# Kernel tuning notes

Measured on AMD Instinct MI355X. Metric: run time of the kernel, lower is better.

Reference implementation:

```python
import jax, jax.numpy as jnp
import numpy as np

B, S, H, NH = 2, 2048, 1024, 16
HD = H // NH  # head_dim = 64


def setup_inputs() -> dict:
    key = jax.random.key(0)
    k1, k2, k3, k4, k5 = jax.random.split(key, 5)
    hidden_states = jax.random.normal(k1, (B, S, H), dtype=jnp.float32)
    # additive causal mask: 0 on/below diagonal, -1e9 above
    causal = jnp.tril(jnp.ones((S, S), dtype=jnp.bool_))
    attention_mask = jnp.where(causal, 0.0, -1e9).astype(jnp.float32)[None, None, :, :]
    scale = 0.02
    Wq = jax.random.normal(k2, (H, H), dtype=jnp.float32) * scale
    Wk = jax.random.normal(k3, (H, H), dtype=jnp.float32) * scale
    Wv = jax.random.normal(k4, (H, H), dtype=jnp.float32) * scale
    Wo = jax.random.normal(k5, (H, H), dtype=jnp.float32) * scale
    return {"hidden_states": hidden_states, "attention_mask": attention_mask,
            "Wq": Wq, "Wk": Wk, "Wv": Wv, "Wo": Wo}


def reference(hidden_states, attention_mask, Wq, Wk, Wv, Wo):
    b, s, _ = hidden_states.shape
    # nn.Linear: y = x @ W.T
    q = (hidden_states @ Wq.T).reshape(b, s, NH, HD).transpose(0, 2, 1, 3)  # [B,NH,S,HD]
    k = (hidden_states @ Wk.T).reshape(b, s, NH, HD).transpose(0, 2, 1, 3)
    v = (hidden_states @ Wv.T).reshape(b, s, NH, HD).transpose(0, 2, 1, 3)
    scores = jnp.einsum('bhqd,bhkd->bhqk', q, k) / jnp.sqrt(jnp.float32(HD))
    scores = scores + attention_mask
    attn = jax.nn.softmax(scores, axis=-1)
    out = jnp.einsum('bhqk,bhkd->bhqd', attn, v)  # [B,NH,S,HD]
    out = out.transpose(0, 2, 1, 3).reshape(b, s, H)
    return out @ Wo.T
```

## Files before the change

kernel.cpp:

```cpp
#include <hip/hip_runtime.h>
#include <hip/hip_bf16.h>

#define B_   2
#define S_   2048
#define H_   1024
#define NH_  16
#define HD_  64
#define MTOT 4096
#define KD   1024

typedef __attribute__((ext_vector_type(4)))  float    f32x4;
typedef __attribute__((ext_vector_type(16))) float    f32x16;
typedef __attribute__((ext_vector_type(8)))  short    bf16x8;
typedef __attribute__((ext_vector_type(2)))  unsigned u32x2;
typedef __attribute__((ext_vector_type(4)))  unsigned u32x4;

__device__ inline short f2bf(float x) {
    union { float f; unsigned u; } v; v.f = x;
    unsigned r = v.u + 0x7fffu + ((v.u >> 16) & 1u);
    return (short)(r >> 16);
}
__device__ inline unsigned pk2(float lo, float hi) {
    return (unsigned)(unsigned short)f2bf(lo) | ((unsigned)(unsigned short)f2bf(hi) << 16);
}
__device__ inline unsigned cvtpk(float lo, float hi) {
    unsigned r;
    asm("v_cvt_pk_bf16_f32 %0, %1, %2" : "=v"(r) : "v"(lo), "v"(hi));
    return r;
}
__device__ inline float max3f(float a, float b, float c) {
    float r;
    asm("v_max3_f32 %0, %1, %2, %3" : "=v"(r) : "v"(a), "v"(b), "v"(c));
    return r;
}
__device__ inline void gload16(const void* g, void* l) {
    __builtin_amdgcn_global_load_lds(
        (const __attribute__((address_space(1))) unsigned*)g,
        (__attribute__((address_space(3))) unsigned*)l, 16, 0, 0);
}

__global__ __launch_bounds__(256) void cvt_x(const float* __restrict__ x,
                                             unsigned* __restrict__ xb) {
    const size_t i = ((size_t)blockIdx.x * 256 + threadIdx.x) * 8;
    const f32x4 a = *(const f32x4*)(x + i);
    const f32x4 b = *(const f32x4*)(x + i + 4);
    u32x4 p;
    p[0] = pk2(a[0], a[1]); p[1] = pk2(a[2], a[3]);
    p[2] = pk2(b[0], b[1]); p[3] = pk2(b[2], b[3]);
    *(u32x4*)(xb + i / 2) = p;
}

__global__ __launch_bounds__(256) void wcvt(const float* __restrict__ W0,
                                            const float* __restrict__ W1,
                                            const float* __restrict__ W2,
                                            const float* __restrict__ W3,
                                            unsigned* __restrict__ wb) {
    const float* W = (blockIdx.y == 0) ? W0 : (blockIdx.y == 1) ? W1
                   : (blockIdx.y == 2) ? W2 : W3;
    const size_t i = ((size_t)blockIdx.x * 256 + threadIdx.x) * 8;
    const f32x4 a = *(const f32x4*)(W + i);
    const f32x4 b = *(const f32x4*)(W + i + 4);
    u32x4 p;
    p[0] = pk2(a[0], a[1]); p[1] = pk2(a[2], a[3]);
    p[2] = pk2(b[0], b[1]); p[3] = pk2(b[2], b[3]);
    *(u32x4*)(wb + (size_t)blockIdx.y * (H_ * KD / 2) + i / 2) = p;
}

template <int MODE>
__global__ __launch_bounds__(256) void gemm_m97(const short* __restrict__ A,
                                                const short* __restrict__ Wb,
                                                short* __restrict__ outb,
                                                float* __restrict__ outf) {
    __shared__ short Sm[128 * 128];
    short* As = Sm;
    short* Bs = Sm + 8192;

    const int tid = threadIdx.x, wave = tid >> 6, lane = tid & 63;
    const int wm = (wave >> 1) * 64, wn = (wave & 1) * 64;
    const int m0 = blockIdx.x * 128;

    int n0, widx;
    if constexpr (MODE == 0) {
        widx = blockIdx.y >> 3;
        n0 = (blockIdx.y & 7) * 128;
    } else {
        widx = 0;
        n0 = blockIdx.y * 128;
    }
    const short* W = Wb + (size_t)widx * H_ * KD;

    f32x4 acc[4][4] = {};

    for (int k0 = 0; k0 < KD; k0 += 64) {
#pragma unroll
        for (int c = 0; c < 4; ++c) {
            const int lin = wave * 4096 + c * 1024 + lane * 16;
            const int row = lin >> 7;
            const int col = (lin & 127) ^ ((row & 7) << 4);
            gload16(A + (size_t)(m0 + row) * KD + k0 + (col >> 1),
                    (char*)As + wave * 4096 + c * 1024);
            gload16(W + (size_t)(n0 + row) * KD + k0 + (col >> 1),
                    (char*)Bs + wave * 4096 + c * 1024);
        }
        __syncthreads();

#pragma unroll
        for (int ks = 0; ks < 2; ++ks) {
            bf16x8 af[4], bf[4];
#pragma unroll
            for (int i = 0; i < 4; ++i) {
                const int row = wm + i * 16 + (lane & 15);
                af[i] = *(const bf16x8*)((char*)As + row * 128 +
                        ((ks * 64 + (lane >> 4) * 16) ^ ((row & 7) << 4)));
            }
#pragma unroll
            for (int j = 0; j < 4; ++j) {
                const int row = wn + j * 16 + (lane & 15);
                bf[j] = *(const bf16x8*)((char*)Bs + row * 128 +
                        ((ks * 64 + (lane >> 4) * 16) ^ ((row & 7) << 4)));
            }
#pragma unroll
            for (int i = 0; i < 4; ++i)
#pragma unroll
                for (int j = 0; j < 4; ++j)
                    acc[i][j] = __builtin_amdgcn_mfma_f32_16x16x32_bf16(af[i], bf[j], acc[i][j], 0, 0, 0);
        }
        __syncthreads();
    }

    if constexpr (MODE == 0) {
#pragma unroll
        for (int i = 0; i < 4; ++i)
#pragma unroll
            for (int j = 0; j < 4; ++j)
#pragma unroll
                for (int r = 0; r < 4; ++r) {
                    const int mi = wm + i * 16 + (lane >> 4) * 4 + r;
                    const int ni = wn + j * 16 + (lane & 15);
                    const int byt = (mi * 256 + ni * 2) ^ ((mi & 7) << 4);
                    *(short*)((char*)Sm + byt) = f2bf(acc[i][j][r]);
                }
        __syncthreads();
        const int row = tid >> 1, half = tid & 1;
        const int m = m0 + row, bb = m >> 11, s = m & 2047;
        const int hh = (n0 >> 6) + half;
        short* dst = outb + (size_t)widx * MTOT * H_ +
                     (((size_t)(bb * NH_ + hh)) * S_ + s) * HD_;
#pragma unroll
        for (int k = 0; k < 8; ++k) {
            const int byt = (row * 256 + half * 128 + k * 16) ^ ((row & 7) << 4);
            *(bf16x8*)(dst + k * 8) = *(const bf16x8*)((char*)Sm + byt);
        }
    } else {
#pragma unroll
        for (int i = 0; i < 4; ++i)
#pragma unroll
            for (int j = 0; j < 4; ++j)
#pragma unroll
                for (int r = 0; r < 4; ++r) {
                    const int m = m0 + wm + i * 16 + (lane >> 4) * 4 + r;
                    const int n = n0 + wn + j * 16 + (lane & 15);
                    outf[(size_t)m * H_ + n] = acc[i][j][r];
                }
    }
}

__global__ __launch_bounds__(512, 4) void flash3(const short* __restrict__ Qb,
                                                 const short* __restrict__ Kb,
                                                 const short* __restrict__ Vb,
                                                 short* __restrict__ Ob) {
    const int bx = blockIdx.x;
    const int hi = bx >> 8, u = bx & 255;
    const int h = u >> 4, tq = u & 15;
    const int qt = hi ? (15 - tq) : tq;
    const int b  = hi;

    const int tid = threadIdx.x, wave = tid >> 6, lane = tid & 63;
    const int qg = wave & 3, half = wave >> 2;
    const int th = tid & 255;
    const int q0 = qt * 128;
    const int qw0 = q0 + qg * 32;
    const size_t hoff = ((size_t)(b * NH_ + h)) * S_ * HD_;
    const short* Q = Qb + hoff;
    const short* K = Kb + hoff;
    const short* V = Vb + hoff;

    __shared__ short Ks[2][2][4096];
    __shared__ short Vt[2][2][4096];

    const int ql = lane & 31;
    const int hh = lane >> 5;

    bf16x8 qf[4];
#pragma unroll
    for (int ds = 0; ds < 4; ++ds)
        qf[ds] = *(const bf16x8*)(Q + (size_t)(qw0 + ql) * HD_ + ds * 16 + hh * 8);

    f32x16 ot[2] = {};
    float mrun = -1e30f, lrun = 0.f;
    const float c2 = 0.18033688011112042f;

    const int kk = (th & 31) * 2, d0v = (th >> 5) * 8;
    bf16x8 vr0, vr1;
    auto stageK = [&](int kt, int buf) {
#pragma unroll
        for (int c = 0; c < 2; ++c) {
            const int lin = qg * 2048 + c * 1024 + lane * 16;
            const int row = lin >> 7;
            const int col = (lin & 127) ^ ((row & 7) << 4);
            gload16(K + (size_t)(kt * 64 + row) * HD_ + (col >> 1),
                    (char*)Ks[half][buf] + qg * 2048 + c * 1024);
        }
    };
    auto loadV = [&](int kt) {
        vr0 = *(const bf16x8*)(V + (size_t)(kt * 64 + kk) * HD_ + d0v);
        vr1 = *(const bf16x8*)(V + (size_t)(kt * 64 + kk + 1) * HD_ + d0v);
    };
    auto writeV = [&](int buf) {
#pragma unroll
        for (int i = 0; i < 8; ++i) {
            const int d = d0v + i;
            const int byt = d * 128 + kk * 2;
            *(unsigned*)((char*)Vt[half][buf] + (byt ^ ((d & 7) << 4))) =
                (unsigned)(unsigned short)vr0[i] | ((unsigned)(unsigned short)vr1[i] << 16);
        }
    };

    const int niter = qt + 1;
    const int ktbase = half ? (qt + 1) : 0;

    stageK(ktbase, 0);
    loadV(ktbase);
    writeV(0);
    __syncthreads();

    int cur = 0;
    for (int it = 0; it < niter; ++it) {
        const int kt = ktbase + it;
        const bool pre = (it + 1 < niter);
        if (pre) { stageK(kt + 1, cur ^ 1); loadV(kt + 1); }

        if (kt * 64 <= qw0 + 31) {
            const bool need_mask = (kt * 64 + 63) > qw0;

            f32x16 st[2] = {};
            __builtin_amdgcn_s_setprio(1);
#pragma unroll
            for (int t = 0; t < 2; ++t)
#pragma unroll
                for (int ds = 0; ds < 4; ++ds) {
                    const int row = t * 32 + ql;
                    const bf16x8 kf = *(const bf16x8*)((char*)Ks[half][cur] + row * 128 +
                            ((ds * 32 + hh * 16) ^ ((row & 7) << 4)));
                    st[t] = __builtin_amdgcn_mfma_f32_32x32x16_bf16(kf, qf[ds], st[t], 0, 0, 0);
                }
            __builtin_amdgcn_s_setprio(0);

            float sraw[32];
#pragma unroll
            for (int t = 0; t < 2; ++t)
#pragma unroll
                for (int r = 0; r < 16; ++r) {
                    float v = st[t][r];
                    if (need_mask) {
                        const int key = kt * 64 + t * 32 + (r & 3) + 8 * (r >> 2) + 4 * hh;
                        if (key > qw0 + ql) v = -1e30f;
                    }
                    sraw[t * 16 + r] = v;
                }

            float ma = fmaxf(sraw[0], sraw[1]);
            float mb = fmaxf(sraw[2], sraw[3]);
#pragma unroll
            for (int i = 4; i < 32; i += 4) {
                ma = max3f(ma, sraw[i],     sraw[i + 1]);
                mb = max3f(mb, sraw[i + 2], sraw[i + 3]);
            }
            const float pmax = fmaxf(fmaxf(ma, mb), __shfl_xor(fmaxf(ma, mb), 32, 64));

            if (!__all((pmax - mrun) <= 44.36f)) {
                const float mnew = fmaxf(mrun, pmax);
                const float corr = exp2f((mrun - mnew) * c2);
                mrun = mnew;
                lrun *= corr;
#pragma unroll
                for (int dt = 0; dt < 2; ++dt)
#pragma unroll
                    for (int r = 0; r < 16; ++r) ot[dt][r] *= corr;
            }
            const float mc = mrun * c2;

            float p[32];
#pragma unroll
            for (int i = 0; i < 32; ++i) p[i] = exp2f(fmaf(sraw[i], c2, -mc));
            float ts[16];
#pragma unroll
            for (int i = 0; i < 16; ++i) ts[i] = p[i] + p[i + 16];
#pragma unroll
            for (int stp = 8; stp >= 1; stp >>= 1)
#pragma unroll
                for (int i = 0; i < 8; ++i)
                    if (i < stp) ts[i] += ts[i + stp];
            lrun += ts[0] + __shfl_xor(ts[0], 32, 64);

#pragma unroll
            for (int ks = 0; ks < 4; ++ks) {
                const int t = ks >> 1, rb = (ks & 1) * 8;
                const unsigned a0 = cvtpk(p[t * 16 + rb + 0], p[t * 16 + rb + 1]);
                const unsigned a1 = cvtpk(p[t * 16 + rb + 2], p[t * 16 + rb + 3]);
                const unsigned a2 = cvtpk(p[t * 16 + rb + 4], p[t * 16 + rb + 5]);
                const unsigned a3 = cvtpk(p[t * 16 + rb + 6], p[t * 16 + rb + 7]);
                const unsigned s0 = __shfl_xor(a0, 32, 64);
                const unsigned s1 = __shfl_xor(a1, 32, 64);
                const unsigned s2 = __shfl_xor(a2, 32, 64);
                const unsigned s3 = __shfl_xor(a3, 32, 64);
                u32x4 pw;
                pw[0] = hh ? s2 : a0;
                pw[1] = hh ? s3 : a1;
                pw[2] = hh ? a2 : s0;
                pw[3] = hh ? a3 : s1;
                const bf16x8 pf = __builtin_bit_cast(bf16x8, pw);
                __builtin_amdgcn_s_setprio(1);
#pragma unroll
                for (int dt = 0; dt < 2; ++dt) {
                    const int row = dt * 32 + ql;
                    const bf16x8 vf = *(const bf16x8*)((char*)Vt[half][cur] + row * 128 +
                            ((ks * 32 + hh * 16) ^ ((row & 7) << 4)));
                    ot[dt] = __builtin_amdgcn_mfma_f32_32x32x16_bf16(vf, pf, ot[dt], 0, 0, 0);
                }
                __builtin_amdgcn_s_setprio(0);
            }
        }

        if (pre) writeV(cur ^ 1);
        __syncthreads();
        cur ^= 1;
    }

    float* Osh = (float*)Ks;
    float* Msh = (float*)Vt;
    const int swz = (lane & 7) << 2;

    if (half == 1) {
        float* dst = Osh + ((size_t)qg * 64 + lane) * 32;
#pragma unroll
        for (int dt = 0; dt < 2; ++dt)
#pragma unroll
            for (int g4 = 0; g4 < 4; ++g4) {
                f32x4 t;
                t[0] = ot[dt][g4 * 4 + 0]; t[1] = ot[dt][g4 * 4 + 1];
                t[2] = ot[dt][g4 * 4 + 2]; t[3] = ot[dt][g4 * 4 + 3];
                *(f32x4*)(dst + ((dt * 16 + g4 * 4) ^ swz)) = t;
            }
        Msh[(qg * 64 + lane) * 2 + 0] = mrun;
        Msh[(qg * 64 + lane) * 2 + 1] = lrun;
    }
    __syncthreads();

    if (half == 0) {
        const float* src = Osh + ((size_t)qg * 64 + lane) * 32;
        const float mB = Msh[(qg * 64 + lane) * 2 + 0];
        const float lB = Msh[(qg * 64 + lane) * 2 + 1];
        const float m  = fmaxf(mrun, mB);
        const float al = exp2f((mrun - m) * c2);
        const float be = exp2f((mB   - m) * c2);
        const float inv = 1.f / (al * lrun + be * lB);
        const float ai = al * inv, bi = be * inv;

        short* orow = Ob + ((size_t)(b * S_) + q0 + qg * 32 + ql) * H_ + h * HD_;
#pragma unroll
        for (int dt = 0; dt < 2; ++dt)
#pragma unroll
            for (int g4 = 0; g4 < 4; ++g4) {
                const f32x4 ob = *(const f32x4*)(src + ((dt * 16 + g4 * 4) ^ swz));
                const int dbase = dt * 32 + 8 * g4 + 4 * hh;
                u32x2 w;
                w[0] = cvtpk(ot[dt][g4 * 4 + 0] * ai + ob[0] * bi,
                             ot[dt][g4 * 4 + 1] * ai + ob[1] * bi);
                w[1] = cvtpk(ot[dt][g4 * 4 + 2] * ai + ob[2] * bi,
                             ot[dt][g4 * 4 + 3] * ai + ob[3] * bi);
                *(u32x2*)(orow + dbase) = w;
            }
    }
}

extern "C" void kernel_launch(void* const* d_in, const int* in_sizes, int n_in,
                              void* d_out, int out_size, void* d_ws, size_t ws_size,
                              hipStream_t stream) {
    const float* x  = (const float*)d_in[0];
    const float* Wq = (const float*)d_in[2];
    const float* Wk = (const float*)d_in[3];
    const float* Wv = (const float*)d_in[4];
    const float* Wo = (const float*)d_in[5];
    float* out = (float*)d_out;

    short* qkv = (short*)d_ws;
    short* xb  = qkv + (size_t)3 * MTOT * H_;
    short* wb  = xb + (size_t)MTOT * H_;

    cvt_x<<<2048, 256, 0, stream>>>(x, (unsigned*)xb);
    wcvt<<<dim3(512, 4), 256, 0, stream>>>(Wq, Wk, Wv, Wo, (unsigned*)wb);

    gemm_m97<0><<<dim3(32, 24), 256, 0, stream>>>(xb, wb, qkv, nullptr);

    flash3<<<dim3(512), 512, 0, stream>>>(
        qkv, qkv + (size_t)MTOT * H_, qkv + (size_t)2 * MTOT * H_, xb);

    gemm_m97<1><<<dim3(32, 8), 256, 0, stream>>>(
        xb, wb + (size_t)3 * H_ * KD, nullptr, out);
}
```

Before: 153.0 us.

## Interleave KV tiles between wave halves instead of contiguous ranges

The two halves of the workgroup previously each walked a contiguous range of KV tiles (first half from 0, second from qt+1). Now each iteration stages a pair of adjacent tiles with all 512 threads cooperating, and the halves take even and odd tiles. The goal is to keep the causal-masked diagonal work balanced between halves and to share the staging load across all waves. It changes which tiles each half covers and how many it visits, so both halves now hit masked and skipped tiles near the diagonal.

```diff
diff --git a/kernel.cpp b/kernel.cpp
--- a/kernel.cpp
+++ b/kernel.cpp
@@ -165,7 +165,7 @@
     }
 }
 
-__global__ __launch_bounds__(512, 4) void flash3(const short* __restrict__ Qb,
+__global__ __launch_bounds__(512, 4) void flash4(const short* __restrict__ Qb,
                                                  const short* __restrict__ Kb,
                                                  const short* __restrict__ Vb,
                                                  short* __restrict__ Ob) {
@@ -176,8 +176,7 @@
     const int b  = hi;
 
     const int tid = threadIdx.x, wave = tid >> 6, lane = tid & 63;
-    const int qg = wave & 3, half = wave >> 2;
-    const int th = tid & 255;
+    const int qg = wave & 3, par = wave >> 2;
     const int q0 = qt * 128;
     const int qw0 = q0 + qg * 32;
     const size_t hoff = ((size_t)(b * NH_ + h)) * S_ * HD_;
@@ -200,46 +199,52 @@
     float mrun = -1e30f, lrun = 0.f;
     const float c2 = 0.18033688011112042f;
 
-    const int kk = (th & 31) * 2, d0v = (th >> 5) * 8;
-    bf16x8 vr0, vr1;
-    auto stageK = [&](int kt, int buf) {
+    auto stagePair = [&](int j) {
+        const int buf = j & 1;
 #pragma unroll
         for (int c = 0; c < 2; ++c) {
-            const int lin = qg * 2048 + c * 1024 + lane * 16;
+            const int chunk = wave * 2 + c;
+            const int pt  = chunk >> 3;
+            const int sub = chunk & 7;
+            const int lin = sub * 1024 + lane * 16;
             const int row = lin >> 7;
             const int col = (lin & 127) ^ ((row & 7) << 4);
-            gload16(K + (size_t)(kt * 64 + row) * HD_ + (col >> 1),
-                    (char*)Ks[half][buf] + qg * 2048 + c * 1024);
+            gload16(K + (size_t)((2 * j + pt) * 64 + row) * HD_ + (col >> 1),
+                    (char*)Ks[pt][buf] + sub * 1024);
         }
     };
-    auto loadV = [&](int kt) {
+    const int vpar = tid >> 8;
+    const int kk = (tid & 31) * 2, d0v = ((tid >> 5) & 7) * 8;
+    bf16x8 vr0, vr1;
+    auto loadV = [&](int j) {
+        const int kt = 2 * j + vpar;
         vr0 = *(const bf16x8*)(V + (size_t)(kt * 64 + kk) * HD_ + d0v);
         vr1 = *(const bf16x8*)(V + (size_t)(kt * 64 + kk + 1) * HD_ + d0v);
     };
-    auto writeV = [&](int buf) {
+    auto writeV = [&](int j) {
+        const int buf = j & 1;
 #pragma unroll
         for (int i = 0; i < 8; ++i) {
             const int d = d0v + i;
             const int byt = d * 128 + kk * 2;
-            *(unsigned*)((char*)Vt[half][buf] + (byt ^ ((d & 7) << 4))) =
+            *(unsigned*)((char*)Vt[vpar][buf] + (byt ^ ((d & 7) << 4))) =
                 (unsigned)(unsigned short)vr0[i] | ((unsigned)(unsigned short)vr1[i] << 16);
         }
     };
 
     const int niter = qt + 1;
-    const int ktbase = half ? (qt + 1) : 0;
-
-    stageK(ktbase, 0);
-    loadV(ktbase);
+
+    stagePair(0);
+    loadV(0);
     writeV(0);
     __syncthreads();
 
-    int cur = 0;
     for (int it = 0; it < niter; ++it) {
-        const int kt = ktbase + it;
         const bool pre = (it + 1 < niter);
-        if (pre) { stageK(kt + 1, cur ^ 1); loadV(kt + 1); }
-
+        if (pre) { stagePair(it + 1); loadV(it + 1); }
+
+        const int kt = 2 * it + par;
+        const int buf = it & 1;
         if (kt * 64 <= qw0 + 31) {
             const bool need_mask = (kt * 64 + 63) > qw0;
 
@@ -250,7 +255,7 @@
 #pragma unroll
                 for (int ds = 0; ds < 4; ++ds) {
                     const int row = t * 32 + ql;
-                    const bf16x8 kf = *(const bf16x8*)((char*)Ks[half][cur] + row * 128 +
+                    const bf16x8 kf = *(const bf16x8*)((char*)Ks[par][buf] + row * 128 +
                             ((ds * 32 + hh * 16) ^ ((row & 7) << 4)));
                     st[t] = __builtin_amdgcn_mfma_f32_32x32x16_bf16(kf, qf[ds], st[t], 0, 0, 0);
                 }
@@ -324,7 +329,7 @@
 #pragma unroll
                 for (int dt = 0; dt < 2; ++dt) {
                     const int row = dt * 32 + ql;
-                    const bf16x8 vf = *(const bf16x8*)((char*)Vt[half][cur] + row * 128 +
+                    const bf16x8 vf = *(const bf16x8*)((char*)Vt[par][buf] + row * 128 +
                             ((ks * 32 + hh * 16) ^ ((row & 7) << 4)));
                     ot[dt] = __builtin_amdgcn_mfma_f32_32x32x16_bf16(vf, pf, ot[dt], 0, 0, 0);
                 }
@@ -332,16 +337,15 @@
             }
         }
 
-        if (pre) writeV(cur ^ 1);
+        if (pre) writeV(it + 1);
         __syncthreads();
-        cur ^= 1;
     }
 
     float* Osh = (float*)Ks;
     float* Msh = (float*)Vt;
     const int swz = (lane & 7) << 2;
 
-    if (half == 1) {
+    if (par == 1) {
         float* dst = Osh + ((size_t)qg * 64 + lane) * 32;
 #pragma unroll
         for (int dt = 0; dt < 2; ++dt)
@@ -357,7 +361,7 @@
     }
     __syncthreads();
 
-    if (half == 0) {
+    if (par == 0) {
         const float* src = Osh + ((size_t)qg * 64 + lane) * 32;
         const float mB = Msh[(qg * 64 + lane) * 2 + 0];
         const float lB = Msh[(qg * 64 + lane) * 2 + 1];
@@ -403,7 +407,7 @@
 
     gemm_m97<0><<<dim3(32, 24), 256, 0, stream>>>(xb, wb, qkv, nullptr);
 
-    flash3<<<dim3(512), 512, 0, stream>>>(
+    flash4<<<dim3(512), 512, 0, stream>>>(
         qkv, qkv + (size_t)MTOT * H_, qkv + (size_t)2 * MTOT * H_, xb);
 
     gemm_m97<1><<<dim3(32, 8), 256, 0, stream>>>(
```

Result: faster. 147.8 us (-3.4%).
